# Kernel optimization log

Measured on AMD Instinct MI355X. Metric: run time of the kernel, lower is better.

The kernel has to match this reference:

```python
import jax, jax.numpy as jnp
import numpy as np

N = 20000
E = 640000
D = 128


def setup_inputs() -> dict:
    key = jax.random.key(0)
    ks = jax.random.split(key, 8)
    x = jax.random.normal(ks[0], (N, D), dtype=jnp.float32)
    edge_index = jax.random.randint(ks[1], (2, E), 0, N, dtype=jnp.int64)
    s = 1.0 / np.sqrt(D)
    inp = {"x": x, "edge_index": edge_index}
    for i, layer in enumerate([2, 4, 6]):
        inp[f"W{i+1}"] = jax.random.uniform(ks[layer], (D, D), jnp.float32, -s, s)
        inp[f"b{i+1}"] = jax.random.uniform(ks[layer + 1], (D,), jnp.float32, -s, s)
    return inp


def _gcn_layer(x, src, dst, deg_inv, W, b):
    # linear (torch convention: y = x @ W.T + b), W: [out, in]
    xt = x @ W.T + b
    # gather source-node features, scatter-mean onto targets
    msg = xt[src]                                   # [E, D]
    agg = jax.ops.segment_sum(msg, dst, num_segments=N)  # [N, D]
    agg = agg * deg_inv[:, None]                    # mean over incoming edges
    return jax.nn.relu(agg) + xt


def reference(x, edge_index, W1, b1, W2, b2, W3, b3):
    src, dst = edge_index[0], edge_index[1]
    deg = jax.ops.segment_sum(jnp.ones((E,), jnp.float32), dst, num_segments=N)
    deg_inv = jnp.where(deg > 0, 1.0 / jnp.maximum(deg, 1.0), 0.0)
    for W, b in ((W1, b1), (W2, b2), (W3, b3)):
        x = _gcn_layer(x, src, dst, deg_inv, W, b)
    return x
```

## Files before the change

### kernel.cpp

```cpp
#include <hip/hip_runtime.h>

#define DD 128
#define KC 32
#define MT 64
#define ELLC 128
#define NBMAX 320
#define ACAP 2304
#define AEPW 4096

__device__ __forceinline__ unsigned f2bf_rne(float f) {
    unsigned u = __float_as_uint(f);
    u += 0x7fffu + ((u >> 16) & 1u);
    return u >> 16;
}

__device__ __forceinline__ void gemm_body(float Xs[KC][MT + 4], float Ws[KC][DD + 4],
                                          const float* x,
                                          const float* __restrict__ W,
                                          const float* __restrict__ b,
                                          float* xt,
                                          unsigned* __restrict__ xtb, int M, int blk) {
    const int tid  = threadIdx.x;
    const int cg   = tid & 15;
    const int rg   = tid >> 4;
    const int row0 = blk * MT;

    float acc[4][8];
#pragma unroll
    for (int i = 0; i < 4; ++i)
#pragma unroll
        for (int j = 0; j < 8; ++j) acc[i][j] = 0.0f;

    for (int kc = 0; kc < DD; kc += KC) {
#pragma unroll
        for (int it = 0; it < 2; ++it) {
            int idx = tid + it * 256;
            int r = idx >> 3, kq = idx & 7;
            int gr = row0 + r;
            float4 v = make_float4(0.f, 0.f, 0.f, 0.f);
            if (gr < M) v = *(const float4*)&x[gr * DD + kc + kq * 4];
            Xs[kq * 4 + 0][r] = v.x; Xs[kq * 4 + 1][r] = v.y;
            Xs[kq * 4 + 2][r] = v.z; Xs[kq * 4 + 3][r] = v.w;
        }
#pragma unroll
        for (int it = 0; it < 4; ++it) {
            int idx = tid + it * 256;
            int o = idx >> 3, kq = idx & 7;
            float4 v = *(const float4*)&W[o * DD + kc + kq * 4];
            Ws[kq * 4 + 0][o] = v.x; Ws[kq * 4 + 1][o] = v.y;
            Ws[kq * 4 + 2][o] = v.z; Ws[kq * 4 + 3][o] = v.w;
        }
        __syncthreads();

#pragma unroll 8
        for (int k = 0; k < KC; ++k) {
            float4 xv = *(const float4*)&Xs[k][rg * 4];
            float4 w0 = *(const float4*)&Ws[k][cg * 8];
            float4 w1 = *(const float4*)&Ws[k][cg * 8 + 4];
            float xr[4] = {xv.x, xv.y, xv.z, xv.w};
            float wc[8] = {w0.x, w0.y, w0.z, w0.w, w1.x, w1.y, w1.z, w1.w};
#pragma unroll
            for (int i = 0; i < 4; ++i)
#pragma unroll
                for (int j = 0; j < 8; ++j) acc[i][j] += xr[i] * wc[j];
        }
        __syncthreads();
    }

    float4 b0 = *(const float4*)&b[cg * 8];
    float4 b1 = *(const float4*)&b[cg * 8 + 4];
    float bb[8] = {b0.x, b0.y, b0.z, b0.w, b1.x, b1.y, b1.z, b1.w};
#pragma unroll
    for (int i = 0; i < 4; ++i) {
        int gr = row0 + rg * 4 + i;
        if (gr < M) {
            float v[8];
#pragma unroll
            for (int j = 0; j < 8; ++j) v[j] = acc[i][j] + bb[j];
            *(float4*)&xt[gr * DD + cg * 8]     = make_float4(v[0], v[1], v[2], v[3]);
            *(float4*)&xt[gr * DD + cg * 8 + 4] = make_float4(v[4], v[5], v[6], v[7]);
            uint4 p;
            p.x = f2bf_rne(v[0]) | (f2bf_rne(v[1]) << 16);
            p.y = f2bf_rne(v[2]) | (f2bf_rne(v[3]) << 16);
            p.z = f2bf_rne(v[4]) | (f2bf_rne(v[5]) << 16);
            p.w = f2bf_rne(v[6]) | (f2bf_rne(v[7]) << 16);
            *(uint4*)&xtb[gr * 64 + cg * 4] = p;
        }
    }
}

__global__ __launch_bounds__(256) void gemm_xwT(const float* x,
                                                const float* __restrict__ W,
                                                const float* __restrict__ b,
                                                float* xt,
                                                unsigned* __restrict__ xtb, int M) {
    __shared__ float Xs[KC][MT + 4];
    __shared__ float Ws[KC][DD + 4];
    gemm_body(Xs, Ws, x, W, b, xt, xtb, M, blockIdx.x);
}

__global__ __launch_bounds__(256) void gemm1_plus_binA(const float* x,
                                                       const float* __restrict__ W,
                                                       const float* __restrict__ b,
                                                       float* xt,
                                                       unsigned* __restrict__ xtb, int M,
                                                       const int* __restrict__ src,
                                                       const int* __restrict__ dst,
                                                       int* __restrict__ bucket_count,
                                                       unsigned* __restrict__ bstore,
                                                       int E, int NB, int PA) {
    __shared__ float Xs[KC][MT + 4];
    __shared__ float Ws[KC][DD + 4];
    __shared__ int hist[NBMAX];
    __shared__ int basec[NBMAX];
    __shared__ int cur[NBMAX];

    if ((int)blockIdx.x >= PA) {
        gemm_body(Xs, Ws, x, W, b, xt, xtb, M, blockIdx.x - PA);
        return;
    }

    const int tid = threadIdx.x;
    for (int i = tid; i < NB; i += 256) hist[i] = 0;
    __syncthreads();

    int dv[16], sv[16];
    const int ebase = blockIdx.x * AEPW;
#pragma unroll
    for (int r = 0; r < 4; ++r) {
        int e = ebase + r * 1024 + tid * 4;
        if (e + 4 <= E) {
            int4 d4 = *(const int4*)&dst[e];
            int4 s4 = *(const int4*)&src[e];
            dv[r*4+0] = d4.x; dv[r*4+1] = d4.y; dv[r*4+2] = d4.z; dv[r*4+3] = d4.w;
            sv[r*4+0] = s4.x; sv[r*4+1] = s4.y; sv[r*4+2] = s4.z; sv[r*4+3] = s4.w;
        } else {
#pragma unroll
            for (int q = 0; q < 4; ++q) {
                int ee = e + q;
                if (ee < E) { dv[r*4+q] = dst[ee]; sv[r*4+q] = src[ee]; }
                else        { dv[r*4+q] = -1;      sv[r*4+q] = 0; }
            }
        }
    }
#pragma unroll
    for (int i = 0; i < 16; ++i)
        if (dv[i] >= 0) atomicAdd(&hist[dv[i] >> 6], 1);
    __syncthreads();

    for (int bk = tid; bk < NB; bk += 256) {
        int h = hist[bk];
        basec[bk] = h ? atomicAdd(&bucket_count[bk], h) : 0;
        cur[bk] = 0;
    }
    __syncthreads();

#pragma unroll
    for (int i = 0; i < 16; ++i) {
        if (dv[i] >= 0) {
            int bk = dv[i] >> 6;
            int pos = basec[bk] + atomicAdd(&cur[bk], 1);
            if (pos < ACAP)
                bstore[bk * ACAP + pos] = ((unsigned)(dv[i] & 63) << 16) | (unsigned)sv[i];
        }
    }
}

__global__ __launch_bounds__(256) void ell_build(const unsigned* __restrict__ bstore,
                                                 const int* __restrict__ bucket_count,
                                                 unsigned short* __restrict__ colell,
                                                 int* __restrict__ deg, int N) {
    __shared__ int c64[64];
    const int bk = blockIdx.x;
    for (int i = threadIdx.x; i < 64; i += 256) c64[i] = 0;
    __syncthreads();
    int cnt = bucket_count[bk];
    if (cnt > ACAP) cnt = ACAP;
    for (int i = threadIdx.x; i < cnt; i += 256) {
        unsigned code = bstore[bk * ACAP + i];
        int local = (int)(code >> 16);
        int s     = (int)(code & 0xffffu);
        int p = atomicAdd(&c64[local], 1);
        if (p < ELLC)
            colell[((((bk << 6) + local)) << 7) + p] = (unsigned short)s;
    }
    __syncthreads();
    if (threadIdx.x < 64) {
        int node = (bk << 6) + threadIdx.x;
        if (node < N) deg[node] = c64[threadIdx.x];
    }
}

__global__ void gcn_aggregate(const uint4* __restrict__ xtb4, const float* xt,
                              const unsigned short* __restrict__ colell,
                              const int* __restrict__ deg,
                              float* out, int N) {
    const int gid  = blockIdx.x * blockDim.x + threadIdx.x;
    const int node = gid >> 6;
    const int lane = threadIdx.x & 63;
    if (node >= N) return;
    const int h  = lane & 15;
    const int qt = lane >> 4;

    const uint4* __restrict__ xl = xtb4 + h;
    const unsigned short* __restrict__ crow = colell + (node << 7);
    const int cnt = deg[node];

    float a0 = 0.f, a1 = 0.f, a2 = 0.f, a3 = 0.f;
    float a4 = 0.f, a5 = 0.f, a6 = 0.f, a7 = 0.f;

#define ACC_U4(u)                                     \
    do {                                              \
        a0 += __uint_as_float((u).x << 16);           \
        a1 += __uint_as_float((u).x & 0xffff0000u);   \
        a2 += __uint_as_float((u).y << 16);           \
        a3 += __uint_as_float((u).y & 0xffff0000u);   \
        a4 += __uint_as_float((u).z << 16);           \
        a5 += __uint_as_float((u).z & 0xffff0000u);   \
        a6 += __uint_as_float((u).w << 16);           \
        a7 += __uint_as_float((u).w & 0xffff0000u);   \
    } while (0)

    for (int base = 0; base < cnt; base += 64) {
        const int rem = cnt - base;
        const int c = rem < 64 ? rem : 64;
        const int myidx = (lane < c) ? (int)crow[base + lane] : 0;
        const int quads = c >> 2;
        int t = 0;
        for (; t + 8 <= quads; t += 8) {
            uint4 u[8];
#pragma unroll
            for (int q = 0; q < 8; ++q) {
                int s = __shfl(myidx, 4 * (t + q) + qt, 64);
                u[q] = xl[s << 4];
            }
#pragma unroll
            for (int q = 0; q < 8; ++q) ACC_U4(u[q]);
        }
        for (; t + 2 <= quads; t += 2) {
            uint4 u0, u1;
            int s0 = __shfl(myidx, 4 * t + qt, 64);
            int s1 = __shfl(myidx, 4 * t + 4 + qt, 64);
            u0 = xl[s0 << 4];
            u1 = xl[s1 << 4];
            ACC_U4(u0);
            ACC_U4(u1);
        }
        for (; t < quads; ++t) {
            int s = __shfl(myidx, 4 * t + qt, 64);
            uint4 u = xl[s << 4];
            ACC_U4(u);
        }
        const int r = c & 3;
        if (r) {
            int eidx = 4 * quads + qt;
            int s = __shfl(myidx, eidx, 64);
            if (eidx < c) {
                uint4 u = xl[s << 4];
                ACC_U4(u);
            }
        }
    }
#undef ACC_U4

    a0 += __shfl_down(a0, 32, 64); a1 += __shfl_down(a1, 32, 64);
    a2 += __shfl_down(a2, 32, 64); a3 += __shfl_down(a3, 32, 64);
    a4 += __shfl_down(a4, 32, 64); a5 += __shfl_down(a5, 32, 64);
    a6 += __shfl_down(a6, 32, 64); a7 += __shfl_down(a7, 32, 64);
    a0 += __shfl_down(a0, 16, 64); a1 += __shfl_down(a1, 16, 64);
    a2 += __shfl_down(a2, 16, 64); a3 += __shfl_down(a3, 16, 64);
    a4 += __shfl_down(a4, 16, 64); a5 += __shfl_down(a5, 16, 64);
    a6 += __shfl_down(a6, 16, 64); a7 += __shfl_down(a7, 16, 64);

    if (lane < 16) {
        const float di = (cnt > 0) ? (1.0f / (float)cnt) : 0.0f;
        float4 t0 = ((const float4*)xt)[node * 32 + h * 2];
        float4 t1 = ((const float4*)xt)[node * 32 + h * 2 + 1];
        float4 o0, o1;
        o0.x = fmaxf(a0 * di, 0.f) + t0.x;
        o0.y = fmaxf(a1 * di, 0.f) + t0.y;
        o0.z = fmaxf(a2 * di, 0.f) + t0.z;
        o0.w = fmaxf(a3 * di, 0.f) + t0.w;
        o1.x = fmaxf(a4 * di, 0.f) + t1.x;
        o1.y = fmaxf(a5 * di, 0.f) + t1.y;
        o1.z = fmaxf(a6 * di, 0.f) + t1.z;
        o1.w = fmaxf(a7 * di, 0.f) + t1.w;
        ((float4*)out)[node * 32 + h * 2]     = o0;
        ((float4*)out)[node * 32 + h * 2 + 1] = o1;
    }
}

extern "C" void kernel_launch(void* const* d_in, const int* in_sizes, int n_in,
                              void* d_out, int out_size, void* d_ws, size_t ws_size,
                              hipStream_t stream) {
    const float* x  = (const float*)d_in[0];
    const int*   ei = (const int*)d_in[1];
    const float* W1 = (const float*)d_in[2];
    const float* b1 = (const float*)d_in[3];
    const float* W2 = (const float*)d_in[4];
    const float* b2 = (const float*)d_in[5];
    const float* W3 = (const float*)d_in[6];
    const float* b3 = (const float*)d_in[7];

    const int N  = in_sizes[0] / DD;
    const int E  = in_sizes[1] / 2;
    const int ND = N * DD;

    const int* src = ei;
    const int* dst = ei + E;

    const int NB = (N + 63) >> 6;
    const int PA = (E + AEPW - 1) / AEPW;
    const int GB = (N + MT - 1) / MT;
    const int AB = (N + 3) / 4;

    char* ws = (char*)d_ws;
    size_t off = 0;
    auto alloc = [&](size_t bytes) {
        void* p = ws + off;
        off += (bytes + 255) & ~(size_t)255;
        return p;
    };
    int*            bucket_count = (int*)alloc((size_t)NB * sizeof(int));
    unsigned*       bstore       = (unsigned*)alloc((size_t)NB * ACAP * sizeof(unsigned));
    unsigned short* colell       = (unsigned short*)alloc((size_t)NB * 64 * ELLC * sizeof(unsigned short));
    int*            deg          = (int*)alloc((size_t)N * sizeof(int));
    unsigned*       xtb          = (unsigned*)alloc((size_t)(ND / 2) * sizeof(unsigned));

    float* xbuf = (float*)d_out;

    hipMemsetAsync(bucket_count, 0, (size_t)NB * sizeof(int), stream);
    gemm1_plus_binA<<<PA + GB, 256, 0, stream>>>(x, W1, b1, xbuf, xtb, N,
                                                 src, dst, bucket_count, bstore, E, NB, PA);
    ell_build<<<NB, 256, 0, stream>>>(bstore, bucket_count, colell, deg, N);

    gcn_aggregate<<<AB, 256, 0, stream>>>((const uint4*)xtb, xbuf, colell, deg, xbuf, N);

    gemm_xwT<<<GB, 256, 0, stream>>>(xbuf, W2, b2, xbuf, xtb, N);
    gcn_aggregate<<<AB, 256, 0, stream>>>((const uint4*)xtb, xbuf, colell, deg, xbuf, N);

    gemm_xwT<<<GB, 256, 0, stream>>>(xbuf, W3, b3, xbuf, xtb, N);
    gcn_aggregate<<<AB, 256, 0, stream>>>((const uint4*)xtb, xbuf, colell, deg, xbuf, N);
}
```

Before: 214.9 us.

## Split bf16 feature table into column halves and aggregate in two passes

```diff
diff --git a/kernel.cpp b/kernel.cpp
--- a/kernel.cpp
+++ b/kernel.cpp
@@ -19,7 +19,8 @@
                                           const float* __restrict__ W,
                                           const float* __restrict__ b,
                                           float* xt,
-                                          unsigned* __restrict__ xtb, int M, int blk) {
+                                          unsigned* __restrict__ xtbA,
+                                          unsigned* __restrict__ xtbB, int M, int blk) {
     const int tid  = threadIdx.x;
     const int cg   = tid & 15;
     const int rg   = tid >> 4;
@@ -70,6 +71,8 @@
     float4 b0 = *(const float4*)&b[cg * 8];
     float4 b1 = *(const float4*)&b[cg * 8 + 4];
     float bb[8] = {b0.x, b0.y, b0.z, b0.w, b1.x, b1.y, b1.z, b1.w};
+    unsigned* __restrict__ tb = (cg < 8) ? xtbA : xtbB;
+    const int tcol = (cg & 7) * 4;
 #pragma unroll
     for (int i = 0; i < 4; ++i) {
         int gr = row0 + rg * 4 + i;
@@ -84,7 +87,7 @@
             p.y = f2bf_rne(v[2]) | (f2bf_rne(v[3]) << 16);
             p.z = f2bf_rne(v[4]) | (f2bf_rne(v[5]) << 16);
             p.w = f2bf_rne(v[6]) | (f2bf_rne(v[7]) << 16);
-            *(uint4*)&xtb[gr * 64 + cg * 4] = p;
+            *(uint4*)&tb[gr * 32 + tcol] = p;
         }
     }
 }
@@ -93,17 +96,19 @@
                                                 const float* __restrict__ W,
                                                 const float* __restrict__ b,
                                                 float* xt,
-                                                unsigned* __restrict__ xtb, int M) {
+                                                unsigned* __restrict__ xtbA,
+                                                unsigned* __restrict__ xtbB, int M) {
     __shared__ float Xs[KC][MT + 4];
     __shared__ float Ws[KC][DD + 4];
-    gemm_body(Xs, Ws, x, W, b, xt, xtb, M, blockIdx.x);
+    gemm_body(Xs, Ws, x, W, b, xt, xtbA, xtbB, M, blockIdx.x);
 }
 
 __global__ __launch_bounds__(256) void gemm1_plus_binA(const float* x,
                                                        const float* __restrict__ W,
                                                        const float* __restrict__ b,
                                                        float* xt,
-                                                       unsigned* __restrict__ xtb, int M,
+                                                       unsigned* __restrict__ xtbA,
+                                                       unsigned* __restrict__ xtbB, int M,
                                                        const int* __restrict__ src,
                                                        const int* __restrict__ dst,
                                                        int* __restrict__ bucket_count,
@@ -116,7 +121,7 @@
     __shared__ int cur[NBMAX];
 
     if ((int)blockIdx.x >= PA) {
-        gemm_body(Xs, Ws, x, W, b, xt, xtb, M, blockIdx.x - PA);
+        gemm_body(Xs, Ws, x, W, b, xt, xtbA, xtbB, M, blockIdx.x - PA);
         return;
     }
 
@@ -191,10 +196,10 @@
     }
 }
 
-__global__ void gcn_aggregate(const uint4* __restrict__ xtb4, const float* xt,
-                              const unsigned short* __restrict__ colell,
-                              const int* __restrict__ deg,
-                              float* out, int N) {
+__global__ void gcn_aggregate_half(const uint2* __restrict__ tb, const float* xt,
+                                   const unsigned short* __restrict__ colell,
+                                   const int* __restrict__ deg,
+                                   float* out, int N, int halfOfs) {
     const int gid  = blockIdx.x * blockDim.x + threadIdx.x;
     const int node = gid >> 6;
     const int lane = threadIdx.x & 63;
@@ -202,23 +207,18 @@
     const int h  = lane & 15;
     const int qt = lane >> 4;
 
-    const uint4* __restrict__ xl = xtb4 + h;
+    const uint2* __restrict__ xl = tb + h;
     const unsigned short* __restrict__ crow = colell + (node << 7);
     const int cnt = deg[node];
 
     float a0 = 0.f, a1 = 0.f, a2 = 0.f, a3 = 0.f;
-    float a4 = 0.f, a5 = 0.f, a6 = 0.f, a7 = 0.f;
-
-#define ACC_U4(u)                                     \
+
+#define ACC_U2(u)                                     \
     do {                                              \
         a0 += __uint_as_float((u).x << 16);           \
         a1 += __uint_as_float((u).x & 0xffff0000u);   \
         a2 += __uint_as_float((u).y << 16);           \
         a3 += __uint_as_float((u).y & 0xffff0000u);   \
-        a4 += __uint_as_float((u).z << 16);           \
-        a5 += __uint_as_float((u).z & 0xffff0000u);   \
-        a6 += __uint_as_float((u).w << 16);           \
-        a7 += __uint_as_float((u).w & 0xffff0000u);   \
     } while (0)
 
     for (int base = 0; base < cnt; base += 64) {
@@ -228,65 +228,47 @@
         const int quads = c >> 2;
         int t = 0;
         for (; t + 8 <= quads; t += 8) {
-            uint4 u[8];
+            uint2 u[8];
 #pragma unroll
             for (int q = 0; q < 8; ++q) {
                 int s = __shfl(myidx, 4 * (t + q) + qt, 64);
                 u[q] = xl[s << 4];
             }
 #pragma unroll
-            for (int q = 0; q < 8; ++q) ACC_U4(u[q]);
-        }
-        for (; t + 2 <= quads; t += 2) {
-            uint4 u0, u1;
-            int s0 = __shfl(myidx, 4 * t + qt, 64);
-            int s1 = __shfl(myidx, 4 * t + 4 + qt, 64);
-            u0 = xl[s0 << 4];
-            u1 = xl[s1 << 4];
-            ACC_U4(u0);
-            ACC_U4(u1);
+            for (int q = 0; q < 8; ++q) ACC_U2(u[q]);
         }
         for (; t < quads; ++t) {
             int s = __shfl(myidx, 4 * t + qt, 64);
-            uint4 u = xl[s << 4];
-            ACC_U4(u);
+            uint2 u = xl[s << 4];
+            ACC_U2(u);
         }
         const int r = c & 3;
         if (r) {
             int eidx = 4 * quads + qt;
             int s = __shfl(myidx, eidx, 64);
-            if (eidx < c) {
-                uint4 u = xl[s << 4];
-                ACC_U4(u);
+            if (qt < r) {
+                uint2 u = xl[s << 4];
+                ACC_U2(u);
             }
         }
     }
-#undef ACC_U4
+#undef ACC_U2
 
     a0 += __shfl_down(a0, 32, 64); a1 += __shfl_down(a1, 32, 64);
     a2 += __shfl_down(a2, 32, 64); a3 += __shfl_down(a3, 32, 64);
-    a4 += __shfl_down(a4, 32, 64); a5 += __shfl_down(a5, 32, 64);
-    a6 += __shfl_down(a6, 32, 64); a7 += __shfl_down(a7, 32, 64);
     a0 += __shfl_down(a0, 16, 64); a1 += __shfl_down(a1, 16, 64);
     a2 += __shfl_down(a2, 16, 64); a3 += __shfl_down(a3, 16, 64);
-    a4 += __shfl_down(a4, 16, 64); a5 += __shfl_down(a5, 16, 64);
-    a6 += __shfl_down(a6, 16, 64); a7 += __shfl_down(a7, 16, 64);
 
     if (lane < 16) {
         const float di = (cnt > 0) ? (1.0f / (float)cnt) : 0.0f;
-        float4 t0 = ((const float4*)xt)[node * 32 + h * 2];
-        float4 t1 = ((const float4*)xt)[node * 32 + h * 2 + 1];
-        float4 o0, o1;
-        o0.x = fmaxf(a0 * di, 0.f) + t0.x;
-        o0.y = fmaxf(a1 * di, 0.f) + t0.y;
-        o0.z = fmaxf(a2 * di, 0.f) + t0.z;
-        o0.w = fmaxf(a3 * di, 0.f) + t0.w;
-        o1.x = fmaxf(a4 * di, 0.f) + t1.x;
-        o1.y = fmaxf(a5 * di, 0.f) + t1.y;
-        o1.z = fmaxf(a6 * di, 0.f) + t1.z;
-        o1.w = fmaxf(a7 * di, 0.f) + t1.w;
-        ((float4*)out)[node * 32 + h * 2]     = o0;
-        ((float4*)out)[node * 32 + h * 2 + 1] = o1;
+        const float4* xr = (const float4*)(xt + node * DD + halfOfs);
+        float4 t4 = xr[h];
+        float4 o;
+        o.x = fmaxf(a0 * di, 0.f) + t4.x;
+        o.y = fmaxf(a1 * di, 0.f) + t4.y;
+        o.z = fmaxf(a2 * di, 0.f) + t4.z;
+        o.w = fmaxf(a3 * di, 0.f) + t4.w;
+        ((float4*)(out + node * DD + halfOfs))[h] = o;
     }
 }
 
@@ -325,20 +307,22 @@
     unsigned*       bstore       = (unsigned*)alloc((size_t)NB * ACAP * sizeof(unsigned));
     unsigned short* colell       = (unsigned short*)alloc((size_t)NB * 64 * ELLC * sizeof(unsigned short));
     int*            deg          = (int*)alloc((size_t)N * sizeof(int));
-    unsigned*       xtb          = (unsigned*)alloc((size_t)(ND / 2) * sizeof(unsigned));
+    unsigned*       xtbA         = (unsigned*)alloc((size_t)N * 32 * sizeof(unsigned));
+    unsigned*       xtbB         = (unsigned*)alloc((size_t)N * 32 * sizeof(unsigned));
 
     float* xbuf = (float*)d_out;
 
-    hipMemsetAsync(bucket_count, 0, (size_t)NB * sizeof(int), stream);
-    gemm1_plus_binA<<<PA + GB, 256, 0, stream>>>(x, W1, b1, xbuf, xtb, N,
+    (void)hipMemsetAsync(bucket_count, 0, (size_t)NB * sizeof(int), stream);
+    gemm1_plus_binA<<<PA + GB, 256, 0, stream>>>(x, W1, b1, xbuf, xtbA, xtbB, N,
                                                  src, dst, bucket_count, bstore, E, NB, PA);
     ell_build<<<NB, 256, 0, stream>>>(bstore, bucket_count, colell, deg, N);
 
-    gcn_aggregate<<<AB, 256, 0, stream>>>((const uint4*)xtb, xbuf, colell, deg, xbuf, N);
-
-    gemm_xwT<<<GB, 256, 0, stream>>>(xbuf, W2, b2, xbuf, xtb, N);
-    gcn_aggregate<<<AB, 256, 0, stream>>>((const uint4*)xtb, xbuf, colell, deg, xbuf, N);
-
-    gemm_xwT<<<GB, 256, 0, stream>>>(xbuf, W3, b3, xbuf, xtb, N);
-    gcn_aggregate<<<AB, 256, 0, stream>>>((const uint4*)xtb, xbuf, colell, deg, xbuf, N);
-}
+    for (int layer = 0; layer < 3; ++layer) {
+        if (layer == 1)
+            gemm_xwT<<<GB, 256, 0, stream>>>(xbuf, W2, b2, xbuf, xtbA, xtbB, N);
+        else if (layer == 2)
+            gemm_xwT<<<GB, 256, 0, stream>>>(xbuf, W3, b3, xbuf, xtbA, xtbB, N);
+        gcn_aggregate_half<<<AB, 256, 0, stream>>>((const uint2*)xtbA, xbuf, colell, deg, xbuf, N, 0);
+        gcn_aggregate_half<<<AB, 256, 0, stream>>>((const uint2*)xtbB, xbuf, colell, deg, xbuf, N, 64);
+    }
+}
```

Measured after the change: 233.6 us. 8.7% more time.
